# Kernel optimization log

Measured on AMD Instinct MI355X. Metric: run time of the kernel, lower is better.

The kernel has to match this reference:

```python
import jax, jax.numpy as jnp
import numpy as np

ALPHA = 0.02
NEG = -9e15

def lrelu(x):
    return jnp.where(x >= 0, x, ALPHA * x)

def layer_norm(x, eps=1e-5):
    m = jnp.mean(x, axis=-1, keepdims=True)
    v = jnp.var(x, axis=-1, keepdims=True)
    return (x - m) * jax.lax.rsqrt(v + eps)

def setup_inputs() -> dict:
    key = jax.random.key(0)
    ks = jax.random.split(key, 10)
    B, N, F_IN, D = 8, 2048, 10, 128
    h = jax.random.normal(ks[0], (B, N, F_IN), jnp.float32)
    adj = jax.random.randint(ks[1], (B, N, N), 0, 2, jnp.int32)
    s = 0.1
    return {
        "h": h,
        "adj": adj,
        "W1": jax.random.normal(ks[2], (D, F_IN), jnp.float32) * s,
        "b1": jax.random.normal(ks[3], (D,), jnp.float32) * s,
        "Wg": jax.random.normal(ks[4], (D, D), jnp.float32) * s,
        "bg": jax.random.normal(ks[5], (D,), jnp.float32) * s,
        "a1": jax.random.normal(ks[6], (D,), jnp.float32) * s,
        "a2": jax.random.normal(ks[7], (D,), jnp.float32) * s,
        "W2": jax.random.normal(ks[8], (2, D), jnp.float32) * s,
        "b2": jax.random.normal(ks[9], (2,), jnp.float32) * s,
    }

def reference(h, adj, W1, b1, Wg, bg, a1, a2, W2, b2):
    # fc1 + layernorm + leakyrelu
    x = h @ W1.T + b1                      # [B,N,128]
    x = lrelu(layer_norm(x))
    # GAT layer
    Wh = x @ Wg.T + bg                     # [B,N,128]
    e1 = Wh @ a1                           # [B,N]
    e2 = Wh @ a2                           # [B,N]
    e = lrelu(e1[:, :, None] + e2[:, None, :])  # [B,N,N]
    e = jnp.where(adj != 0, e, NEG)
    attn = jax.nn.softmax(e, axis=2)
    hp = jnp.einsum('bij,bjd->bid', attn, Wh)    # [B,N,128]
    hp = lrelu(layer_norm(hp))
    # global max pool over nodes
    pooled = jnp.max(hp, axis=1)           # [B,128]
    out = pooled @ W2.T + b2               # [B,2]
    return jax.nn.log_softmax(out, axis=-1)
```

## Files before the change

kernel.cpp:

```cpp
#include <hip/hip_runtime.h>

#define B 8
#define N 2048
#define FIN 10
#define D 128
#define ALPHA 0.02f
#define BR 32
#define TI 32
#define JC 128
#define NBLK_ATTN ((N / TI) * B)

typedef short bf8 __attribute__((ext_vector_type(8)));
typedef short s4v __attribute__((ext_vector_type(4)));
typedef float f32x4 __attribute__((ext_vector_type(4)));

__device__ __forceinline__ float lrelu(float x) { return x >= 0.f ? x : ALPHA * x; }

__device__ __forceinline__ short f2b(float f) {
    unsigned u = __float_as_uint(f);
    return (short)((u + 0x7fffu + ((u >> 16) & 1u)) >> 16);
}

__device__ __forceinline__ unsigned enc_key(float v) {
    unsigned b = __float_as_uint(v);
    return (b & 0x80000000u) ? ~b : (b | 0x80000000u);
}
__device__ __forceinline__ float dec_key(unsigned k) {
    unsigned b = (k & 0x80000000u) ? (k & 0x7fffffffu) : ~k;
    return __uint_as_float(b);
}

__global__ __launch_bounds__(256) void k_proj(
    const float* __restrict__ h, const float* __restrict__ W1, const float* __restrict__ b1,
    const float* __restrict__ Wg, const float* __restrict__ bg,
    const float* __restrict__ a1, const float* __restrict__ a2,
    unsigned short* __restrict__ WhT, float* __restrict__ e1g, float* __restrict__ e2g,
    unsigned* __restrict__ pooled, unsigned* __restrict__ cnt)
{
    __shared__ __align__(16) short xep_lds[32 * 136];
    __shared__ __align__(16) short wg_lds[D * 136];
    __shared__ float W1_lds[D * 11];
    __shared__ float h_lds[BR * FIN];
    __shared__ float ep1[2][BR], ep2[2][BR];

    const int t = threadIdx.x;
    const int r0 = blockIdx.x * BR;
    const int bb = r0 >> 11;
    const int jloc = r0 & (N - 1);

    if (blockIdx.x < B && t < D) pooled[blockIdx.x * D + t] = 0u;
    if (blockIdx.x == 0 && t == 128) *cnt = 0u;

    for (int idx = t; idx < D * FIN; idx += 256)
        W1_lds[(idx / FIN) * 11 + (idx % FIN)] = W1[idx];
    for (int idx = t; idx < BR * FIN; idx += 256)
        h_lds[idx] = h[(size_t)r0 * FIN + idx];
    __syncthreads();

    {
        const int dr = t >> 4;
        const int j8 = t & 15;
        #pragma unroll
        for (int pass = 0; pass < 8; pass++) {
            int dd = pass * 16 + dr;
            float4 f0 = *(const float4*)&Wg[dd * D + j8 * 8];
            float4 f1 = *(const float4*)&Wg[dd * D + j8 * 8 + 4];
            bf8 v;
            v[0] = f2b(f0.x); v[1] = f2b(f0.y); v[2] = f2b(f0.z); v[3] = f2b(f0.w);
            v[4] = f2b(f1.x); v[5] = f2b(f1.y); v[6] = f2b(f1.z); v[7] = f2b(f1.w);
            *(bf8*)&wg_lds[dd * 136 + j8 * 8] = v;
        }
    }

    const int w = t >> 6, lane = t & 63;
    {
        float b1v0 = b1[lane], b1v1 = b1[lane + 64];
        for (int i = 0; i < 8; i++) {
            int r = w * 8 + i;
            float s0 = b1v0, s1 = b1v1;
            const float* hr = &h_lds[r * FIN];
            #pragma unroll
            for (int k = 0; k < FIN; k++) {
                float hv = hr[k];
                s0 += hv * W1_lds[lane * 11 + k];
                s1 += hv * W1_lds[(lane + 64) * 11 + k];
            }
            float sm = s0 + s1, sq = s0 * s0 + s1 * s1;
            #pragma unroll
            for (int m = 1; m <= 32; m <<= 1) { sm += __shfl_xor(sm, m); sq += __shfl_xor(sq, m); }
            float mean = sm * (1.f / D);
            float var  = sq * (1.f / D) - mean * mean;
            float rs = rsqrtf(var + 1e-5f);
            xep_lds[r * 136 + lane]      = f2b(lrelu((s0 - mean) * rs));
            xep_lds[r * 136 + lane + 64] = f2b(lrelu((s1 - mean) * rs));
        }
    }
    __syncthreads();

    const int l15 = lane & 15, q = lane >> 4;
    const int mw = w & 1, np = w >> 1;
    f32x4 acc[4];
    #pragma unroll
    for (int nt = 0; nt < 4; nt++)
        #pragma unroll
        for (int r = 0; r < 4; r++) acc[nt][r] = 0.f;

    #pragma unroll
    for (int ks = 0; ks < 4; ks++) {
        bf8 av = *(const bf8*)&xep_lds[(mw * 16 + l15) * 136 + ks * 32 + q * 8];
        #pragma unroll
        for (int nt = 0; nt < 4; nt++) {
            bf8 bv = *(const bf8*)&wg_lds[((np * 4 + nt) * 16 + l15) * 136 + ks * 32 + q * 8];
            acc[nt] = __builtin_amdgcn_mfma_f32_16x16x32_bf16(av, bv, acc[nt], 0, 0, 0);
        }
    }

    float e1p[4] = {0.f, 0.f, 0.f, 0.f}, e2p[4] = {0.f, 0.f, 0.f, 0.f};
    #pragma unroll
    for (int nt = 0; nt < 4; nt++) {
        int col = (np * 4 + nt) * 16 + l15;
        float bgv = bg[col], a1v = a1[col], a2v = a2[col];
        #pragma unroll
        for (int r = 0; r < 4; r++) {
            float v = acc[nt][r] + bgv;
            acc[nt][r] = v;
            e1p[r] += v * a1v;
            e2p[r] += v * a2v;
        }
    }
    #pragma unroll
    for (int m = 1; m <= 8; m <<= 1) {
        #pragma unroll
        for (int r = 0; r < 4; r++) { e1p[r] += __shfl_xor(e1p[r], m); e2p[r] += __shfl_xor(e2p[r], m); }
    }
    if (l15 == 0) {
        #pragma unroll
        for (int r = 0; r < 4; r++) {
            ep1[np][mw * 16 + q * 4 + r] = e1p[r];
            ep2[np][mw * 16 + q * 4 + r] = e2p[r];
        }
    }
    __syncthreads();
    if (t < BR) {
        e1g[r0 + t] = ep1[0][t] + ep1[1][t];
        e2g[r0 + t] = ep2[0][t] + ep2[1][t];
    }
    #pragma unroll
    for (int nt = 0; nt < 4; nt++) {
        int col = (np * 4 + nt) * 16 + l15;
        #pragma unroll
        for (int r = 0; r < 4; r++)
            xep_lds[col * 36 + mw * 16 + q * 4 + r] = f2b(acc[nt][r]);
    }
    __syncthreads();
    {
        const int col = t >> 1, jh = (t & 1) * 16;
        unsigned short* dst = WhT + ((size_t)(bb * D + col)) * N + jloc + jh;
        #pragma unroll
        for (int i2 = 0; i2 < 4; i2++)
            *(uint2*)(dst + i2 * 4) = *(const uint2*)&xep_lds[col * 36 + jh + i2 * 4];
    }
}

__global__ __launch_bounds__(512) void k_attn(
    const int* __restrict__ adj, const unsigned short* __restrict__ WhT,
    const float* __restrict__ e1g, const float* __restrict__ e2g,
    unsigned* __restrict__ pooled, unsigned* __restrict__ cnt,
    const float* __restrict__ W2, const float* __restrict__ b2,
    float* __restrict__ out)
{
    __shared__ __align__(16) short pT[TI * 136];
    __shared__ __align__(16) short whT[D * 136];
    __shared__ float statsp[4][TI][2];
    __shared__ float maxb[2][D];
    __shared__ int finalflag;

    const int t = threadIdx.x;
    const int b = blockIdx.y;
    const int i0 = blockIdx.x * TI;

    const int w = t >> 6, lane = t & 63;
    const int l15 = lane & 15, q = lane >> 4;
    const int mw = w & 1;
    const int np = w >> 1;

    const int rg = t >> 5;
    const int jq = (t & 31) * 4;
    const int dr = t >> 4;
    const int j8 = t & 15;

    const float e1r0 = e1g[b * N + i0 + rg * 2];
    const float e1r1 = e1g[b * N + i0 + rg * 2 + 1];

    const unsigned short* WhTb = WhT + (size_t)b * D * N;
    const int* adjb = adj + ((size_t)b * N + i0) * N;

    f32x4 acc[2], accl;
    #pragma unroll
    for (int nt = 0; nt < 2; nt++)
        #pragma unroll
        for (int r = 0; r < 4; r++) acc[nt][r] = 0.f;
    #pragma unroll
    for (int r = 0; r < 4; r++) accl[r] = 0.f;

    bf8 ones;
    #pragma unroll
    for (int i = 0; i < 8; i++) ones[i] = (short)0x3F80;

    int4 a0 = *(const int4*)(adjb + (size_t)(rg * 2) * N + jq);
    int4 a1r = *(const int4*)(adjb + (size_t)(rg * 2 + 1) * N + jq);
    float4 e2r = *(const float4*)&e2g[b * N + jq];
    bf8 wr0 = *(const bf8*)(WhTb + (size_t)(0 * 32 + dr) * N + j8 * 8);
    bf8 wr1 = *(const bf8*)(WhTb + (size_t)(1 * 32 + dr) * N + j8 * 8);
    bf8 wr2 = *(const bf8*)(WhTb + (size_t)(2 * 32 + dr) * N + j8 * 8);
    bf8 wr3 = *(const bf8*)(WhTb + (size_t)(3 * 32 + dr) * N + j8 * 8);

    for (int jc = 0; jc < N / JC; jc++) {
        {
            s4v pv;
            pv[0] = f2b(a0.x ? __expf(lrelu(e1r0 + e2r.x)) : 0.f);
            pv[1] = f2b(a0.y ? __expf(lrelu(e1r0 + e2r.y)) : 0.f);
            pv[2] = f2b(a0.z ? __expf(lrelu(e1r0 + e2r.z)) : 0.f);
            pv[3] = f2b(a0.w ? __expf(lrelu(e1r0 + e2r.w)) : 0.f);
            *(s4v*)&pT[(rg * 2) * 136 + jq] = pv;
            pv[0] = f2b(a1r.x ? __expf(lrelu(e1r1 + e2r.x)) : 0.f);
            pv[1] = f2b(a1r.y ? __expf(lrelu(e1r1 + e2r.y)) : 0.f);
            pv[2] = f2b(a1r.z ? __expf(lrelu(e1r1 + e2r.z)) : 0.f);
            pv[3] = f2b(a1r.w ? __expf(lrelu(e1r1 + e2r.w)) : 0.f);
            *(s4v*)&pT[(rg * 2 + 1) * 136 + jq] = pv;
            *(bf8*)&whT[(0 * 32 + dr) * 136 + j8 * 8] = wr0;
            *(bf8*)&whT[(1 * 32 + dr) * 136 + j8 * 8] = wr1;
            *(bf8*)&whT[(2 * 32 + dr) * 136 + j8 * 8] = wr2;
            *(bf8*)&whT[(3 * 32 + dr) * 136 + j8 * 8] = wr3;
        }
        __syncthreads();

        if (jc < N / JC - 1) {
            const int j0n = (jc + 1) * JC;
            a0  = *(const int4*)(adjb + (size_t)(rg * 2) * N + j0n + jq);
            a1r = *(const int4*)(adjb + (size_t)(rg * 2 + 1) * N + j0n + jq);
            e2r = *(const float4*)&e2g[b * N + j0n + jq];
            wr0 = *(const bf8*)(WhTb + (size_t)(0 * 32 + dr) * N + j0n + j8 * 8);
            wr1 = *(const bf8*)(WhTb + (size_t)(1 * 32 + dr) * N + j0n + j8 * 8);
            wr2 = *(const bf8*)(WhTb + (size_t)(2 * 32 + dr) * N + j0n + j8 * 8);
            wr3 = *(const bf8*)(WhTb + (size_t)(3 * 32 + dr) * N + j0n + j8 * 8);
        }

        #pragma unroll
        for (int ks = 0; ks < 4; ks++) {
            bf8 av = *(const bf8*)&pT[(mw * 16 + l15) * 136 + ks * 32 + q * 8];
            #pragma unroll
            for (int nt = 0; nt < 2; nt++) {
                bf8 bv = *(const bf8*)&whT[((np * 2 + nt) * 16 + l15) * 136 + ks * 32 + q * 8];
                acc[nt] = __builtin_amdgcn_mfma_f32_16x16x32_bf16(av, bv, acc[nt], 0, 0, 0);
            }
            accl = __builtin_amdgcn_mfma_f32_16x16x32_bf16(av, ones, accl, 0, 0, 0);
        }
        __syncthreads();
    }

    float smr[4] = {0.f, 0.f, 0.f, 0.f}, sqr[4] = {0.f, 0.f, 0.f, 0.f};
    #pragma unroll
    for (int r = 0; r < 4; r++) {
        float rinv = 1.f / accl[r];
        #pragma unroll
        for (int nt = 0; nt < 2; nt++) {
            float v = acc[nt][r] * rinv;
            acc[nt][r] = v;
            smr[r] += v;
            sqr[r] += v * v;
        }
    }
    #pragma unroll
    for (int m = 1; m <= 8; m <<= 1) {
        #pragma unroll
        for (int r = 0; r < 4; r++) { smr[r] += __shfl_xor(smr[r], m); sqr[r] += __shfl_xor(sqr[r], m); }
    }
    if (l15 == 0) {
        #pragma unroll
        for (int r = 0; r < 4; r++) {
            statsp[np][mw * 16 + q * 4 + r][0] = smr[r];
            statsp[np][mw * 16 + q * 4 + r][1] = sqr[r];
        }
    }
    __syncthreads();

    float mx[2] = {-1e30f, -1e30f};
    #pragma unroll
    for (int r = 0; r < 4; r++) {
        int row = mw * 16 + q * 4 + r;
        float s0 = statsp[0][row][0] + statsp[1][row][0] + statsp[2][row][0] + statsp[3][row][0];
        float s1 = statsp[0][row][1] + statsp[1][row][1] + statsp[2][row][1] + statsp[3][row][1];
        float mean = s0 * (1.f / D);
        float var  = s1 * (1.f / D) - mean * mean;
        float rs = rsqrtf(var + 1e-5f);
        #pragma unroll
        for (int nt = 0; nt < 2; nt++) {
            float v = lrelu((acc[nt][r] - mean) * rs);
            mx[nt] = fmaxf(mx[nt], v);
        }
    }
    #pragma unroll
    for (int m = 16; m <= 32; m <<= 1) {
        #pragma unroll
        for (int nt = 0; nt < 2; nt++) mx[nt] = fmaxf(mx[nt], __shfl_xor(mx[nt], m));
    }
    if (q == 0) {
        #pragma unroll
        for (int nt = 0; nt < 2; nt++) maxb[mw][(np * 2 + nt) * 16 + l15] = mx[nt];
    }
    __syncthreads();
    if (t < D) {
        float v = fmaxf(maxb[0][t], maxb[1][t]);
        atomicMax(&pooled[b * D + t], enc_key(v));
    }
    __syncthreads();

    if (t == 0) {
        __threadfence();
        unsigned old = atomicAdd(cnt, 1u);
        finalflag = (old == NBLK_ATTN - 1) ? 1 : 0;
    }
    __syncthreads();
    if (finalflag && t < 256) {
        const int fb = t >> 5;
        const int fq = t & 31;
        float s0 = 0.f, s1 = 0.f;
        #pragma unroll
        for (int m = 0; m < 4; m++) {
            int dd = fq + 32 * m;
            unsigned key = __hip_atomic_load(&pooled[fb * D + dd], __ATOMIC_RELAXED,
                                             __HIP_MEMORY_SCOPE_AGENT);
            float v = dec_key(key);
            s0 += v * W2[dd];
            s1 += v * W2[D + dd];
        }
        #pragma unroll
        for (int m = 1; m <= 16; m <<= 1) { s0 += __shfl_xor(s0, m); s1 += __shfl_xor(s1, m); }
        if (fq == 0) {
            float o0 = s0 + b2[0], o1 = s1 + b2[1];
            float mxv = fmaxf(o0, o1);
            float ls = logf(__expf(o0 - mxv) + __expf(o1 - mxv));
            out[fb * 2 + 0] = o0 - mxv - ls;
            out[fb * 2 + 1] = o1 - mxv - ls;
        }
    }
}

extern "C" void kernel_launch(void* const* d_in, const int* in_sizes, int n_in,
                              void* d_out, int out_size, void* d_ws, size_t ws_size,
                              hipStream_t stream) {
    const float* h   = (const float*)d_in[0];
    const int*   adj = (const int*)d_in[1];
    const float* W1  = (const float*)d_in[2];
    const float* b1  = (const float*)d_in[3];
    const float* Wg  = (const float*)d_in[4];
    const float* bg  = (const float*)d_in[5];
    const float* a1  = (const float*)d_in[6];
    const float* a2  = (const float*)d_in[7];
    const float* W2  = (const float*)d_in[8];
    const float* b2  = (const float*)d_in[9];
    float* out = (float*)d_out;

    unsigned short* WhT = (unsigned short*)d_ws;
    float* e1g = (float*)((char*)d_ws + (size_t)B * D * N * 2);
    float* e2g = e1g + (size_t)B * N;
    unsigned* pooled = (unsigned*)(e2g + (size_t)B * N);
    unsigned* cnt = pooled + (size_t)B * D;

    k_proj<<<(B * N) / BR, 256, 0, stream>>>(h, W1, b1, Wg, bg, a1, a2,
                                             WhT, e1g, e2g, pooled, cnt);
    k_attn<<<dim3(N / TI, B), 512, 0, stream>>>(adj, WhT, e1g, e2g, pooled, cnt,
                                                W2, b2, out);
}
```

Before: 237.8 us.

## Load WhT MFMA operands straight from global and double-buffer the P tile

The WhT B-operand fragments are now read directly from global memory into registers in MFMA layout, so the whT shared-memory staging and its store/load traffic go away. The P tile is double-buffered in LDS, which leaves one barrier per chunk instead of two. The softmax row sums are no longer computed by an extra MFMA against a ones vector; they are accumulated on the VALU from the rounded bf16 values and reduced with shuffles at the end. The cost is WhT loads that each wave issues on demand, less coalesced and no longer prefetched a chunk ahead, which may expose global latency.

```diff
diff --git a/kernel.cpp b/kernel.cpp
--- a/kernel.cpp
+++ b/kernel.cpp
@@ -19,6 +19,10 @@
 __device__ __forceinline__ short f2b(float f) {
     unsigned u = __float_as_uint(f);
     return (short)((u + 0x7fffu + ((u >> 16) & 1u)) >> 16);
+}
+
+__device__ __forceinline__ float b2f(short s) {
+    return __uint_as_float(((unsigned)(unsigned short)s) << 16);
 }
 
 __device__ __forceinline__ unsigned enc_key(float v) {
@@ -169,10 +173,10 @@
     const float* __restrict__ W2, const float* __restrict__ b2,
     float* __restrict__ out)
 {
-    __shared__ __align__(16) short pT[TI * 136];
-    __shared__ __align__(16) short whT[D * 136];
+    __shared__ __align__(16) short pT[2][TI * 136];
     __shared__ float statsp[4][TI][2];
     __shared__ float maxb[2][D];
+    __shared__ float l_lds[TI];
     __shared__ int finalflag;
 
     const int t = threadIdx.x;
@@ -186,83 +190,78 @@
 
     const int rg = t >> 5;
     const int jq = (t & 31) * 4;
-    const int dr = t >> 4;
-    const int j8 = t & 15;
 
     const float e1r0 = e1g[b * N + i0 + rg * 2];
     const float e1r1 = e1g[b * N + i0 + rg * 2 + 1];
 
     const unsigned short* WhTb = WhT + (size_t)b * D * N;
     const int* adjb = adj + ((size_t)b * N + i0) * N;
-
-    f32x4 acc[2], accl;
+    const unsigned short* wrow0 = WhTb + (size_t)((np * 2 + 0) * 16 + l15) * N + q * 8;
+    const unsigned short* wrow1 = WhTb + (size_t)((np * 2 + 1) * 16 + l15) * N + q * 8;
+
+    f32x4 acc[2];
     #pragma unroll
     for (int nt = 0; nt < 2; nt++)
         #pragma unroll
         for (int r = 0; r < 4; r++) acc[nt][r] = 0.f;
-    #pragma unroll
-    for (int r = 0; r < 4; r++) accl[r] = 0.f;
-
-    bf8 ones;
-    #pragma unroll
-    for (int i = 0; i < 8; i++) ones[i] = (short)0x3F80;
+    float ls0 = 0.f, ls1 = 0.f;
 
     int4 a0 = *(const int4*)(adjb + (size_t)(rg * 2) * N + jq);
     int4 a1r = *(const int4*)(adjb + (size_t)(rg * 2 + 1) * N + jq);
     float4 e2r = *(const float4*)&e2g[b * N + jq];
-    bf8 wr0 = *(const bf8*)(WhTb + (size_t)(0 * 32 + dr) * N + j8 * 8);
-    bf8 wr1 = *(const bf8*)(WhTb + (size_t)(1 * 32 + dr) * N + j8 * 8);
-    bf8 wr2 = *(const bf8*)(WhTb + (size_t)(2 * 32 + dr) * N + j8 * 8);
-    bf8 wr3 = *(const bf8*)(WhTb + (size_t)(3 * 32 + dr) * N + j8 * 8);
 
     for (int jc = 0; jc < N / JC; jc++) {
+        bf8 bv0[4], bv1[4];
+        #pragma unroll
+        for (int ks = 0; ks < 4; ks++) {
+            bv0[ks] = *(const bf8*)(wrow0 + jc * JC + ks * 32);
+            bv1[ks] = *(const bf8*)(wrow1 + jc * JC + ks * 32);
+        }
+
+        short* pTc = &pT[jc & 1][0];
+
         {
             s4v pv;
             pv[0] = f2b(a0.x ? __expf(lrelu(e1r0 + e2r.x)) : 0.f);
             pv[1] = f2b(a0.y ? __expf(lrelu(e1r0 + e2r.y)) : 0.f);
             pv[2] = f2b(a0.z ? __expf(lrelu(e1r0 + e2r.z)) : 0.f);
             pv[3] = f2b(a0.w ? __expf(lrelu(e1r0 + e2r.w)) : 0.f);
-            *(s4v*)&pT[(rg * 2) * 136 + jq] = pv;
+            ls0 += b2f(pv[0]) + b2f(pv[1]) + b2f(pv[2]) + b2f(pv[3]);
+            *(s4v*)&pTc[(rg * 2) * 136 + jq] = pv;
             pv[0] = f2b(a1r.x ? __expf(lrelu(e1r1 + e2r.x)) : 0.f);
             pv[1] = f2b(a1r.y ? __expf(lrelu(e1r1 + e2r.y)) : 0.f);
             pv[2] = f2b(a1r.z ? __expf(lrelu(e1r1 + e2r.z)) : 0.f);
             pv[3] = f2b(a1r.w ? __expf(lrelu(e1r1 + e2r.w)) : 0.f);
-            *(s4v*)&pT[(rg * 2 + 1) * 136 + jq] = pv;
-            *(bf8*)&whT[(0 * 32 + dr) * 136 + j8 * 8] = wr0;
-            *(bf8*)&whT[(1 * 32 + dr) * 136 + j8 * 8] = wr1;
-            *(bf8*)&whT[(2 * 32 + dr) * 136 + j8 * 8] = wr2;
-            *(bf8*)&whT[(3 * 32 + dr) * 136 + j8 * 8] = wr3;
-        }
-        __syncthreads();
+            ls1 += b2f(pv[0]) + b2f(pv[1]) + b2f(pv[2]) + b2f(pv[3]);
+            *(s4v*)&pTc[(rg * 2 + 1) * 136 + jq] = pv;
+        }
 
         if (jc < N / JC - 1) {
             const int j0n = (jc + 1) * JC;
             a0  = *(const int4*)(adjb + (size_t)(rg * 2) * N + j0n + jq);
             a1r = *(const int4*)(adjb + (size_t)(rg * 2 + 1) * N + j0n + jq);
             e2r = *(const float4*)&e2g[b * N + j0n + jq];
-            wr0 = *(const bf8*)(WhTb + (size_t)(0 * 32 + dr) * N + j0n + j8 * 8);
-            wr1 = *(const bf8*)(WhTb + (size_t)(1 * 32 + dr) * N + j0n + j8 * 8);
-            wr2 = *(const bf8*)(WhTb + (size_t)(2 * 32 + dr) * N + j0n + j8 * 8);
-            wr3 = *(const bf8*)(WhTb + (size_t)(3 * 32 + dr) * N + j0n + j8 * 8);
-        }
+        }
+
+        __syncthreads();
 
         #pragma unroll
         for (int ks = 0; ks < 4; ks++) {
-            bf8 av = *(const bf8*)&pT[(mw * 16 + l15) * 136 + ks * 32 + q * 8];
-            #pragma unroll
-            for (int nt = 0; nt < 2; nt++) {
-                bf8 bv = *(const bf8*)&whT[((np * 2 + nt) * 16 + l15) * 136 + ks * 32 + q * 8];
-                acc[nt] = __builtin_amdgcn_mfma_f32_16x16x32_bf16(av, bv, acc[nt], 0, 0, 0);
-            }
-            accl = __builtin_amdgcn_mfma_f32_16x16x32_bf16(av, ones, accl, 0, 0, 0);
-        }
-        __syncthreads();
-    }
+            bf8 av = *(const bf8*)&pTc[(mw * 16 + l15) * 136 + ks * 32 + q * 8];
+            acc[0] = __builtin_amdgcn_mfma_f32_16x16x32_bf16(av, bv0[ks], acc[0], 0, 0, 0);
+            acc[1] = __builtin_amdgcn_mfma_f32_16x16x32_bf16(av, bv1[ks], acc[1], 0, 0, 0);
+        }
+    }
+
+    #pragma unroll
+    for (int m = 1; m <= 16; m <<= 1) { ls0 += __shfl_xor(ls0, m); ls1 += __shfl_xor(ls1, m); }
+    if ((t & 31) == 0) { l_lds[rg * 2] = ls0; l_lds[rg * 2 + 1] = ls1; }
+    __syncthreads();
 
     float smr[4] = {0.f, 0.f, 0.f, 0.f}, sqr[4] = {0.f, 0.f, 0.f, 0.f};
     #pragma unroll
     for (int r = 0; r < 4; r++) {
-        float rinv = 1.f / accl[r];
+        float rinv = 1.f / l_lds[mw * 16 + q * 4 + r];
         #pragma unroll
         for (int nt = 0; nt < 2; nt++) {
             float v = acc[nt][r] * rinv;
```

Result: slower. 255.3 us (+7.4%).
